# Kernel optimization log

Hardware: AMD Instinct MI355X
Metric: run time of the kernel (lower is better)

The kernel has to match this reference:

```python
import jax, jax.numpy as jnp
import numpy as np

B, T, J, V, D, H = 32, 400, 30, 50000, 150, 150
L = 2  # answer_token_len (boundary model: start, end)


def _gru_step(h, x, Wih, Whh, bih, bhh):
    # torch GRUCell semantics
    gi = x @ Wih.T + bih
    gh = h @ Whh.T + bhh
    ir, iz, inn = jnp.split(gi, 3, axis=-1)
    hr, hz, hn = jnp.split(gh, 3, axis=-1)
    r = jax.nn.sigmoid(ir + hr)
    z = jax.nn.sigmoid(iz + hz)
    n = jnp.tanh(inn + r * hn)
    return (1.0 - z) * n + z * h


def _gru_seq(x, Wih, Whh, bih, bhh):
    # x: [B, S, din] -> hidden sequence [B, S, h]
    h0 = jnp.zeros((x.shape[0], Whh.shape[1]), x.dtype)
    def step(h, xt):
        h = _gru_step(h, xt, Wih, Whh, bih, bhh)
        return h, h
    _, hs = jax.lax.scan(step, h0, jnp.swapaxes(x, 0, 1))
    return jnp.swapaxes(hs, 0, 1)


def _forward(context, query,
             E,
             ctx_Wih, ctx_Whh, ctx_bih, ctx_bhh,
             q_Wih, q_Whh, q_bih, q_bhh,
             Wq, Wp, Wr, w, gate_bias, attn_bias,
             m_Wih, m_Whh, m_bih, m_bhh,
             mr_Wih, mr_Whh, mr_bih, mr_bhh,
             ptr_W1, ptr_W2, ptr_v,
             d_Wih, d_Whh, d_bih, d_bhh):
    # encode context and query with GRUs
    Hp = _gru_seq(E[context], ctx_Wih, ctx_Whh, ctx_bih, ctx_bhh)  # [B,T,H]
    Hq = _gru_seq(E[query], q_Wih, q_Whh, q_bih, q_bhh)            # [B,J,H]

    whq = jnp.einsum('bjh,hk->bjk', Hq, Wq)  # precomputed query projection [B,J,H]

    def match_scan(xs, cWih, cWhh, cbih, cbhh):
        # xs: [B,T,H] context encodings (possibly time-reversed)
        def step(h, xt):
            # G_i = tanh(Wq Hq + (Wp p_i + Wr h_{i-1}) + bias)  -> [B,J,H]
            g = jnp.tanh(whq + (xt @ Wp + h @ Wr + gate_bias)[:, None, :])
            a = jax.nn.softmax(g @ w + attn_bias, axis=-1)       # [B,J]
            q = jnp.einsum('bj,bjh->bh', a, Hq)                  # attended query
            z = jnp.concatenate([xt, q], axis=-1)                # [B,2H]
            h = _gru_step(h, z, cWih, cWhh, cbih, cbhh)
            return h, h
        h0 = jnp.zeros((xs.shape[0], xs.shape[2]), xs.dtype)
        _, hs = jax.lax.scan(step, h0, jnp.swapaxes(xs, 0, 1))
        return jnp.swapaxes(hs, 0, 1)  # [B,T,H]

    Hf = match_scan(Hp, m_Wih, m_Whh, m_bih, m_bhh)              # forward direction
    Hb = match_scan(Hp[:, ::-1], mr_Wih, mr_Whh, mr_bih, mr_bhh) # reverse direction (scan order, as original)
    Hr = jnp.concatenate([Hf, Hb], axis=-1)                      # [B,T,2H]
    zero0 = jnp.zeros((Hr.shape[0], 1, Hr.shape[2]), Hr.dtype)   # initial zero state prepended
    Hr = jnp.concatenate([zero0, Hr], axis=1)                    # [B,T+1,2H]

    # boundary pointer network: L attention steps over H_r
    enc = Hr @ ptr_W1
    def ptr_step(h, _):
        s = jnp.tanh(enc + (h @ ptr_W2)[:, None, :]) @ ptr_v     # [B,T+1]
        a = jax.nn.softmax(s, axis=-1)
        c = jnp.einsum('bt,bth->bh', a, Hr)
        h = _gru_step(h, c, d_Wih, d_Whh, d_bih, d_bhh)
        return h, a
    h0 = jnp.zeros((Hr.shape[0], Hr.shape[2]), Hr.dtype)
    _, probs = jax.lax.scan(ptr_step, h0, None, length=L)
    return jnp.swapaxes(probs, 0, 1)  # [B, L, T+1]


def setup_inputs() -> dict:
    key = jax.random.key(0)
    keys = iter(jax.random.split(key, 40))
    p = lambda *s: jax.random.normal(next(keys), s, jnp.float32) * 0.05
    inp = {
        'context': jax.random.randint(next(keys), (B, T), 0, V, dtype=jnp.int32),
        'query': jax.random.randint(next(keys), (B, J), 0, V, dtype=jnp.int32),
        'E': p(V, D),
        'ctx_Wih': p(3 * H, D), 'ctx_Whh': p(3 * H, H), 'ctx_bih': p(3 * H), 'ctx_bhh': p(3 * H),
        'q_Wih': p(3 * H, D), 'q_Whh': p(3 * H, H), 'q_bih': p(3 * H), 'q_bhh': p(3 * H),
        'Wq': p(H, H), 'Wp': p(H, H), 'Wr': p(H, H), 'w': p(H),
        'gate_bias': p(H), 'attn_bias': p(),
        'm_Wih': p(3 * H, 2 * H), 'm_Whh': p(3 * H, H), 'm_bih': p(3 * H), 'm_bhh': p(3 * H),
        'mr_Wih': p(3 * H, 2 * H), 'mr_Whh': p(3 * H, H), 'mr_bih': p(3 * H), 'mr_bhh': p(3 * H),
        'ptr_W1': p(2 * H, 2 * H), 'ptr_W2': p(2 * H, 2 * H), 'ptr_v': p(2 * H),
        'd_Wih': p(6 * H, 2 * H), 'd_Whh': p(6 * H, 2 * H), 'd_bih': p(6 * H), 'd_bhh': p(6 * H),
    }
    return inp


def reference(context, query, E,
              ctx_Wih, ctx_Whh, ctx_bih, ctx_bhh,
              q_Wih, q_Whh, q_bih, q_bhh,
              Wq, Wp, Wr, w, gate_bias, attn_bias,
              m_Wih, m_Whh, m_bih, m_bhh,
              mr_Wih, mr_Whh, mr_bih, mr_bhh,
              ptr_W1, ptr_W2, ptr_v,
              d_Wih, d_Whh, d_bih, d_bhh):
    return _forward(context, query, E,
                    ctx_Wih, ctx_Whh, ctx_bih, ctx_bhh,
                    q_Wih, q_Whh, q_bih, q_bhh,
                    Wq, Wp, Wr, w, gate_bias, attn_bias,
                    m_Wih, m_Whh, m_bih, m_bhh,
                    mr_Wih, mr_Whh, mr_bih, mr_bhh,
                    ptr_W1, ptr_W2, ptr_v,
                    d_Wih, d_Whh, d_bih, d_bhh)
```

## Files before the change

### kernel.cpp

```cpp
#include <hip/hip_runtime.h>
#include <hip/hip_bf16.h>


namespace {

constexpr int NBATCH = 32;
constexpr int TLEN   = 400;
constexpr int JQ     = 30;
constexpr int T1     = 401;

__device__ __forceinline__ float sigm(float x){ return 1.f/(1.f+__expf(-x)); }
__device__ __forceinline__ float tanh_f(float x){
  float e = __expf(-2.f*fabsf(x));
  float t = (1.f-e)/(1.f+e);
  return x < 0.f ? -t : t;
}
__device__ __forceinline__ float bf2f(unsigned short u){
  union { unsigned int i; float f; } c; c.i = ((unsigned int)u)<<16; return c.f;
}

#define NW 29
struct WDesc { const void* src[NW]; int off[NW+1]; };

__global__ void sniff_kernel(const unsigned int* __restrict__ bits, int* __restrict__ flag){
  __shared__ int cnt;
  if (threadIdx.x==0) cnt = 0;
  __syncthreads();
  int hit = 0;
  #pragma unroll
  for (int i=0;i<4;i++){
    unsigned int w = bits[threadIdx.x*4+i];
    unsigned int b = (w>>8)&0x7Fu;
    if (b==0u || (b>=0x38u && b<=0x3Fu)) hit++;
  }
  atomicAdd(&cnt, hit);
  __syncthreads();
  if (threadIdx.x==0) *flag = (cnt > 768) ? 1 : 0;
}

__global__ void convert_weights_kernel(WDesc d, float* __restrict__ out, const int* __restrict__ flag){
  const int isbf = *flag;
  const int total = d.off[NW];
  for (int e = blockIdx.x*blockDim.x+threadIdx.x; e < total; e += gridDim.x*blockDim.x){
    int j = 0;
    while (e >= d.off[j+1]) j++;
    int i = e - d.off[j];
    out[e] = isbf ? bf2f(((const unsigned short*)d.src[j])[i])
                  : ((const float*)d.src[j])[i];
  }
}

__global__ void padrows_kernel(const float* __restrict__ src, float* __restrict__ dst,
                               int rows, int cols, int ldd){
  int i = blockIdx.x*blockDim.x+threadIdx.x;
  if (i >= rows*ldd) return;
  int r = i/ldd, c = i-r*ldd;
  dst[i] = (c<cols) ? src[(size_t)r*cols+c] : 0.f;
}

__global__ void transpose_kernel(const float* __restrict__ src, float* __restrict__ dst,
                                 int R, int C, int lds_, int offs){
  int idx = blockIdx.x*blockDim.x+threadIdx.x;
  if (idx >= R*C) return;
  int i = idx / R, k = idx - i*R;
  dst[(size_t)i*R + k] = src[(size_t)k*lds_ + offs + i];
}

__global__ void build_wcat_kernel(const float* __restrict__ Whh, const float* __restrict__ Wr,
                                  float* __restrict__ Wcat){
  int i = blockIdx.x*blockDim.x+threadIdx.x;
  if (i >= 600*152) return;
  int r = i/152, c = i-r*152;
  float v = 0.f;
  if (c < 150){
    if (r < 450) v = Whh[(size_t)r*150+c];
    else         v = Wr[(size_t)c*150 + (r-450)];
  }
  Wcat[i] = v;
}

__global__ void build_msplit_kernel(const float* __restrict__ Wcat,
                                    float* __restrict__ s2q, float* __restrict__ ext){
  int i = blockIdx.x*blockDim.x+threadIdx.x;
  if (i < 24576){
    int q = i/2048, rem = i-q*2048, r = rem/4, p = rem-r*4;
    s2q[i] = Wcat[(size_t)r*152 + 104 + 4*q + p];
  } else if (i < 24576+13376){
    int k = i-24576;
    int q = k/352, rem = k-q*352, ii = rem/4, p = rem-ii*4;
    ext[k] = Wcat[(size_t)(512+ii)*152 + 4*q + p];
  }
}

__global__ void build_gsplit_kernel(const float* __restrict__ Wpad, float* __restrict__ s2q){
  int i = blockIdx.x*blockDim.x+threadIdx.x;
  if (i >= 12*452*4) return;
  int q = i/1808, rem = i-q*1808, r = rem/4, p = rem-r*4;
  s2q[i] = (r<450) ? Wpad[(size_t)r*152 + 104 + 4*q + p] : 0.f;
}

__global__ __launch_bounds__(512) void rowproj16_kernel(
    const float* __restrict__ Xrows,
    const int* __restrict__ gather, const void* __restrict__ Etab, const int* __restrict__ bfflag,
    const float* __restrict__ W, const float* __restrict__ bias,
    float* __restrict__ out, int rows, int K, int inner, int ldw, int ldo)
{
  __shared__ __align__(16) float xs[16][304];
  const int r0 = blockIdx.x*16;
  int nr = rows - r0; if (nr > 16) nr = 16;
  if (nr <= 0) return;
  const int isbf = gather ? *bfflag : 0;
  for (int e = threadIdx.x; e < nr*inner; e += 512){
    int r = e/inner, i = e - r*inner;
    float v;
    if (gather){
      size_t base = (size_t)gather[r0+r]*inner + i;
      v = isbf ? bf2f(((const unsigned short*)Etab)[base]) : ((const float*)Etab)[base];
    } else {
      v = Xrows[(size_t)(r0+r)*inner + i];
    }
    xs[r][i] = v;
  }
  __syncthreads();
  for (int k = threadIdx.x; k < K; k += 512){
    float b0 = bias ? bias[k] : 0.f;
    float acc[16];
    #pragma unroll
    for (int r=0;r<16;r++) acc[r] = b0;
    int i = 0;
    for (; i+4 <= inner; i += 4){
      float w0 = W[(size_t)i*ldw + k];
      float w1 = W[(size_t)(i+1)*ldw + k];
      float w2 = W[(size_t)(i+2)*ldw + k];
      float w3 = W[(size_t)(i+3)*ldw + k];
      #pragma unroll
      for (int r=0;r<16;r++){
        float4 xv = *(const float4*)&xs[r][i];
        acc[r] = fmaf(xv.x, w0, acc[r]);
        acc[r] = fmaf(xv.y, w1, acc[r]);
        acc[r] = fmaf(xv.z, w2, acc[r]);
        acc[r] = fmaf(xv.w, w3, acc[r]);
      }
    }
    for (; i < inner; i++){
      float wv = W[(size_t)i*ldw + k];
      #pragma unroll
      for (int r=0;r<16;r++) acc[r] = fmaf(xs[r][i], wv, acc[r]);
    }
    for (int r=0;r<nr;r++) out[(size_t)(r0+r)*ldo + k] = acc[r];
  }
  for (int k = K + threadIdx.x; k < ldo; k += 512)
    for (int r=0;r<nr;r++) out[(size_t)(r0+r)*ldo + k] = 0.f;
}

#define R26(M) M(0) M(1) M(2) M(3) M(4) M(5) M(6) M(7) M(8) M(9) M(10) M(11) \
               M(12) M(13) M(14) M(15) M(16) M(17) M(18) M(19) M(20) M(21) \
               M(22) M(23) M(24) M(25)
#define DECW(i) float4 w##i;
#define LDW(i)  w##i = wrow4[i];
#define FMAW(i) { float4 hq = h4[i]; \
  acc0 = fmaf(hq.x, w##i.x, acc0); acc1 = fmaf(hq.y, w##i.y, acc1); \
  acc0 = fmaf(hq.z, w##i.z, acc0); acc1 = fmaf(hq.w, w##i.w, acc1); }

__global__ __launch_bounds__(512) void gru_scan_kernel(
    const float* __restrict__ gi0, const float* __restrict__ Wp0,
    const float* __restrict__ s2q0, const float* __restrict__ bh0,
    float* __restrict__ H0, int S0,
    const float* __restrict__ gi1, const float* __restrict__ Wp1,
    const float* __restrict__ s2q1, const float* __restrict__ bh1,
    float* __restrict__ H1, int S1)
{
  const int blk = blockIdx.x;
  const float* gi; const float* Wpad; const float* s2qG; const float* bh; float* Hs; int S;
  if (blk < 32){ gi = gi0 + (size_t)blk*S0*450;  Wpad = Wp0; s2qG = s2q0; bh = bh0;
                 Hs = H0 + (size_t)blk*S0*150;   S = S0; }
  else         { int bb = blk-32;
                 gi = gi1 + (size_t)bb*S1*450;   Wpad = Wp1; s2qG = s2q1; bh = bh1;
                 Hs = H1 + (size_t)bb*S1*150;    S = S1; }
  __shared__ float4 s2W[12*452];
  __shared__ __align__(16) float h[152];
  __shared__ float gh[452];
  const int tid = threadIdx.x;

  R26(DECW)
  float br = 0.f;
  {
    const float4* wrow4 = (const float4*)(Wpad + (size_t)((tid<450)?tid:0)*152);
    R26(LDW)
    if (tid<450) br = bh[tid];
  }
  for (int e=tid; e<12*452; e+=512) s2W[e] = ((const float4*)s2qG)[e];
  if (tid < 152) h[tid] = 0.f;
  __syncthreads();
  const float4* h4 = (const float4*)h;

  for (int t=0;t<S;t++){
    float g0=0.f,g1=0.f,g2=0.f;
    if (tid < 150){
      const float* gg = gi + (size_t)t*450;
      g0 = gg[tid]; g1 = gg[150+tid]; g2 = gg[300+tid];
    }
    if (tid < 450){
      float acc0=br, acc1=0.f;
      R26(FMAW)
      #pragma unroll
      for (int q=0;q<12;q++){
        float4 wq = s2W[q*452+tid]; float4 hq = h4[26+q];
        acc0 = fmaf(hq.x, wq.x, acc0); acc1 = fmaf(hq.y, wq.y, acc1);
        acc0 = fmaf(hq.z, wq.z, acc0); acc1 = fmaf(hq.w, wq.w, acc1);
      }
      gh[tid] = acc0+acc1;
    }
    __syncthreads();
    if (tid < 150){
      float r = sigm(g0 + gh[tid]);
      float z = sigm(g1 + gh[150+tid]);
      float n = tanh_f(g2 + r*gh[300+tid]);
      float hn = (1.f-z)*n + z*h[tid];
      h[tid] = hn;
      Hs[(size_t)t*150 + tid] = hn;
    }
    __syncthreads();
  }
}

__global__ void zero_hr0_kernel(float* __restrict__ Hr){
  int idx = blockIdx.x*blockDim.x + threadIdx.x;
  if (idx < NBATCH*300){
    int b = idx/300, k = idx - 300*b;
    Hr[(size_t)b*T1*300 + k] = 0.f;
  }
}

__global__ __launch_bounds__(512) void match_scan_kernel(
    const float* __restrict__ pWp,
    const float* __restrict__ whq,
    const float* __restrict__ giXf,
    const float* __restrict__ giXr,
    const float* __restrict__ Pf,
    const float* __restrict__ Pr,
    const float* __restrict__ WcatF, const float* __restrict__ WcatR,
    const float* __restrict__ s2qF,  const float* __restrict__ s2qR,
    const float* __restrict__ extF,  const float* __restrict__ extR,
    const float* __restrict__ m_bhh, const float* __restrict__ mr_bhh,
    const float* __restrict__ wvec,
    float* __restrict__ Hr)
{
  const int b   = blockIdx.x;
  const int dir = blockIdx.y;
  const float* giX  = dir ? giXr : giXf;
  const float* P    = dir ? Pr   : Pf;
  const float* Wcat = dir ? WcatR : WcatF;
  const float* s2qG = dir ? s2qR  : s2qF;
  const float* extG = dir ? extR  : extF;
  const float* bhh  = dir ? mr_bhh : m_bhh;

  __shared__ float4 s2W[6144];
  __shared__ float4 extW[3344];
  __shared__ __align__(16) float wrP[760];
  __shared__ __align__(16) float h[152];
  __shared__ float ghsRaw[512];
  __shared__ __align__(16) float gis[452];
  __shared__ __align__(16) float pwS[152];
  __shared__ __align__(16) float wlS[152];
  __shared__ float sc[32], attw[32];

  const int tid  = threadIdx.x;
  const int lane = tid & 63;
  const int wv   = tid >> 6;
  const int er   = (tid < 440) ? (tid % 88) : 0;
  const int kg   = (tid < 440) ? (tid / 88) : 0;

  R26(DECW)
  float br;
  {
    const float4* wrow4 = (const float4*)(Wcat + (size_t)tid*152);
    R26(LDW)
    br = (tid < 450) ? bhh[tid] : 0.f;
  }
  for (int e=tid; e<6144; e+=512) s2W[e]  = ((const float4*)s2qG)[e];
  for (int e=tid; e<3344; e+=512) extW[e] = ((const float4*)extG)[e];
  if (tid < 760) wrP[tid] = 0.f;
  if (tid < 152){
    h[tid] = 0.f;
    wlS[tid] = (tid<150) ? wvec[tid] : 0.f;
  }
  __syncthreads();
  const float4* h4 = (const float4*)h;
  const float4* wrP4 = (const float4*)wrP;

  for (int t=0;t<TLEN;t++){
    const int tt = dir ? (TLEN-1-t) : t;

    float gv = 0.f;
    if (tid < 452) gv = giX[((size_t)b*TLEN + tt)*452 + tid];
    float4 pwv;
    if (tid >= 440 && tid < 478)
      pwv = ((const float4*)(pWp + ((size_t)b*TLEN + tt)*152))[tid-440];

    {
      float acc0=br, acc1=0.f;
      R26(FMAW)
      #pragma unroll
      for (int q=0;q<12;q++){
        float4 wq = s2W[q*512+tid]; float4 hq = h4[26+q];
        acc0 = fmaf(hq.x, wq.x, acc0); acc1 = fmaf(hq.y, wq.y, acc1);
        acc0 = fmaf(hq.z, wq.z, acc0); acc1 = fmaf(hq.w, wq.w, acc1);
      }
      float v = acc0+acc1;
      ghsRaw[tid] = v;
      if (tid >= 450) wrP[tid-450] = v;
    }
    if (tid < 440){
      float e0=0.f, e1=0.f;
      #pragma unroll
      for (int j=0;j<8;j++){
        int q = kg*8+j;
        if (q < 38){
          float4 wq = extW[q*88+er]; float4 hq = h4[q];
          e0 = fmaf(hq.x,wq.x,e0); e1 = fmaf(hq.y,wq.y,e1);
          e0 = fmaf(hq.z,wq.z,e0); e1 = fmaf(hq.w,wq.w,e1);
        }
      }
      wrP[kg*152 + 62 + er] = e0+e1;
    }
    if (tid >= 440 && tid < 478) ((float4*)pwS)[tid-440] = pwv;
    __syncthreads();

    {
      float4 b4; b4.x=b4.y=b4.z=b4.w=0.f;
      const bool bl = (lane < 38);
      if (bl){
        float4 pw4 = ((const float4*)pwS)[lane];
        float4 s0 = wrP4[lane],        s1 = wrP4[38+lane];
        float4 s2 = wrP4[76+lane],     s3 = wrP4[114+lane];
        float4 s4 = wrP4[152+lane];
        b4.x = pw4.x + s0.x+s1.x+s2.x+s3.x+s4.x;
        b4.y = pw4.y + s0.y+s1.y+s2.y+s3.y+s4.y;
        b4.z = pw4.z + s0.z+s1.z+s2.z+s3.z+s4.z;
        b4.w = pw4.w + s0.w+s1.w+s2.w+s3.w+s4.w;
      }
      #pragma unroll
      for (int jj=0;jj<4;jj++){
        int j = wv + 8*jj;
        float a = 0.f;
        if (j < JQ && bl){
          float4 q4 = ((const float4*)(whq + ((size_t)b*JQ + j)*152))[lane];
          float4 w4 = ((const float4*)wlS)[lane];
          a = w4.x*tanh_f(q4.x+b4.x);
          a = fmaf(w4.y, tanh_f(q4.y+b4.y), a);
          a = fmaf(w4.z, tanh_f(q4.z+b4.z), a);
          a = fmaf(w4.w, tanh_f(q4.w+b4.w), a);
        }
        #pragma unroll
        for (int off=32; off; off>>=1) a += __shfl_down(a, off);
        if (j < JQ && lane==0) sc[j] = a;
      }
    }
    __syncthreads();

    if (tid < 64){
      float v = (tid < JQ) ? sc[tid] : -1e30f;
      float m = v;
      #pragma unroll
      for (int off=32; off; off>>=1) m = fmaxf(m, __shfl_down(m, off));
      m = __shfl(m, 0);
      float e = (tid < JQ) ? __expf(v-m) : 0.f;
      float su = e;
      #pragma unroll
      for (int off=32; off; off>>=1) su += __shfl_down(su, off);
      su = __shfl(su, 0);
      if (tid < JQ) attw[tid] = e/su;
    }
    __syncthreads();

    if (tid < 452){
      float acc = gv;
      const float* Pb = P + (size_t)b*JQ*452 + tid;
      #pragma unroll 6
      for (int j=0;j<JQ;j++)
        acc = fmaf(attw[j], Pb[(size_t)j*452], acc);
      gis[tid] = acc;
    }
    __syncthreads();

    if (tid < 150){
      float r = sigm(gis[tid] + ghsRaw[tid]);
      float z = sigm(gis[150+tid] + ghsRaw[150+tid]);
      float n = tanh_f(gis[300+tid] + r*ghsRaw[300+tid]);
      float hn = (1.f-z)*n + z*h[tid];
      h[tid] = hn;
      Hr[((size_t)b*T1 + (t+1))*300 + dir*150 + tid] = hn;
    }
    __syncthreads();
  }
}

__global__ __launch_bounds__(512,2) void ptr_scan_kernel(
    const float* __restrict__ enc, const float* __restrict__ Hr,
    const float* __restrict__ W2, const float* __restrict__ pv,
    const float* __restrict__ dWih, const float* __restrict__ dWhh,
    const float* __restrict__ dbih, const float* __restrict__ dbhh,
    void* __restrict__ outv, const int* __restrict__ flag)
{
  const int b = blockIdx.x;
  const int tid = threadIdx.x;
  const int isbf = *flag;
  __shared__ float h[300], hW2[300], sl[T1], al[T1], c[300];
  __shared__ float gis[900], ghs[900];
  __shared__ float vl[300];
  __shared__ float red[8];
  if (tid < 300){ h[tid] = 0.f; vl[tid] = pv[tid]; }
  __syncthreads();
  for (int l=0;l<2;l++){
    if (tid < 300){
      float a0=0.f,a1=0.f;
      for (int i=0;i<300;i+=2){
        a0 += h[i]  *W2[(size_t)i*300+tid];
        a1 += h[i+1]*W2[(size_t)(i+1)*300+tid];
      }
      hW2[tid] = a0+a1;
    }
    __syncthreads();
    {
      const int wv = tid>>6, lane = tid&63;
      for (int t=wv; t<T1; t+=8){
        const float* er = enc + ((size_t)b*T1 + t)*300;
        float acc = 0.f;
        for (int k=lane; k<300; k+=64) acc += vl[k]*tanh_f(er[k] + hW2[k]);
        #pragma unroll
        for (int off=32; off; off>>=1) acc += __shfl_down(acc, off);
        if (lane==0) sl[t] = acc;
      }
    }
    __syncthreads();
    {
      float v = (tid < T1) ? sl[tid] : -1e30f;
      float m = v;
      #pragma unroll
      for (int off=32; off; off>>=1) m = fmaxf(m, __shfl_down(m, off));
      if ((tid&63)==0) red[tid>>6] = m;
      __syncthreads();
      float bm = fmaxf(fmaxf(fmaxf(red[0],red[1]),fmaxf(red[2],red[3])),
                       fmaxf(fmaxf(red[4],red[5]),fmaxf(red[6],red[7])));
      float e = (tid < T1) ? __expf(v-bm) : 0.f;
      float su = e;
      #pragma unroll
      for (int off=32; off; off>>=1) su += __shfl_down(su, off);
      __syncthreads();
      if ((tid&63)==0) red[tid>>6] = su;
      __syncthreads();
      float bs = red[0]+red[1]+red[2]+red[3]+red[4]+red[5]+red[6]+red[7];
      if (tid < T1){
        float a = e/bs;
        al[tid] = a;
        size_t oi = ((size_t)b*2 + l)*T1 + tid;
        if (isbf) ((__hip_bfloat16*)outv)[oi] = __float2bfloat16(a);
        else      ((float*)outv)[oi] = a;
      }
    }
    __syncthreads();
    if (tid < 300){
      float acc = 0.f;
      for (int t=0;t<T1;t++) acc += al[t]*Hr[((size_t)b*T1 + t)*300 + tid];
      c[tid] = acc;
    }
    __syncthreads();
    for (int k=tid; k<900; k+=blockDim.x){
      const float* wi = dWih + (size_t)k*300;
      const float* wh = dWhh + (size_t)k*300;
      float a0 = dbih[k], a1 = dbhh[k];
      for (int i=0;i<300;i++){ a0 += c[i]*wi[i]; a1 += h[i]*wh[i]; }
      gis[k] = a0; ghs[k] = a1;
    }
    __syncthreads();
    if (tid < 300){
      float r = sigm(gis[tid] + ghs[tid]);
      float z = sigm(gis[300+tid] + ghs[300+tid]);
      float n = tanh_f(gis[600+tid] + r*ghs[600+tid]);
      h[tid] = (1.f-z)*n + z*h[tid];
    }
    __syncthreads();
  }
}

}

extern "C" void kernel_launch(void* const* d_in, const int* in_sizes, int n_in,
                              void* d_out, int out_size, void* d_ws, size_t ws_size,
                              hipStream_t stream)
{
  (void)in_sizes; (void)n_in; (void)out_size; (void)ws_size;
  float* ws = (float*)d_ws;
  int* flag = (int*)d_ws;

  static const int wsz[NW] = {
    67500,67500,450,450,
    67500,67500,450,450,
    22500,22500,22500,150,150,1,
    135000,67500,450,450,
    135000,67500,450,450,
    90000,90000,300,
    270000,270000,900,900
  };
  WDesc desc;
  int cum = 0;
  for (int j=0;j<NW;j++){ desc.src[j] = d_in[3+j]; desc.off[j] = cum; cum += wsz[j]; }
  desc.off[NW] = cum;

  float* WB = ws + 16;
  const float* P_ctx_Wih = WB + desc.off[0];
  const float* P_ctx_Whh = WB + desc.off[1];
  const float* P_ctx_bih = WB + desc.off[2];
  const float* P_ctx_bhh = WB + desc.off[3];
  const float* P_q_Wih   = WB + desc.off[4];
  const float* P_q_Whh   = WB + desc.off[5];
  const float* P_q_bih   = WB + desc.off[6];
  const float* P_q_bhh   = WB + desc.off[7];
  const float* P_Wq      = WB + desc.off[8];
  const float* P_Wp      = WB + desc.off[9];
  const float* P_Wr      = WB + desc.off[10];
  const float* P_w       = WB + desc.off[11];
  const float* P_gb      = WB + desc.off[12];
  const float* P_m_Wih   = WB + desc.off[14];
  const float* P_m_Whh   = WB + desc.off[15];
  const float* P_m_bih   = WB + desc.off[16];
  const float* P_m_bhh   = WB + desc.off[17];
  const float* P_mr_Wih  = WB + desc.off[18];
  const float* P_mr_Whh  = WB + desc.off[19];
  const float* P_mr_bih  = WB + desc.off[20];
  const float* P_mr_bhh  = WB + desc.off[21];
  const float* P_W1      = WB + desc.off[22];
  const float* P_W2      = WB + desc.off[23];
  const float* P_pv      = WB + desc.off[24];
  const float* P_dWih    = WB + desc.off[25];
  const float* P_dWhh    = WB + desc.off[26];
  const float* P_dbih    = WB + desc.off[27];
  const float* P_dbhh    = WB + desc.off[28];

  size_t p = 16 + 1468512;
  float* ctxWhhP = ws + p; p += 68400;
  float* qWhhP   = ws + p; p += 68400;
  float* s2qCtx  = ws + p; p += 21696;
  float* s2qQ    = ws + p; p += 21696;
  float* WcatF   = ws + p; p += 91200;
  float* WcatR   = ws + p; p += 91200;
  float* s2qF    = ws + p; p += 24576;
  float* s2qR    = ws + p; p += 24576;
  float* extFg   = ws + p; p += 13376;
  float* extRg   = ws + p; p += 13376;
  float* ctxWihT = ws + p; p += 67500;
  float* qWihT   = ws + p; p += 67500;
  float* mXfT    = ws + p; p += 67500;
  float* mXrT    = ws + p; p += 67500;
  float* mQfT    = ws + p; p += 67500;
  float* mQrT    = ws + p; p += 67500;

  float* ctx_gi = ws + p; p += 5760000;
  float* q_gi   = ws + p; p += 432000;
  float* HpB    = ws + p; p += 1920000;
  float* HqB    = ws + p; p += 144000;
  float* whqB   = ws + p; p += 145920;
  float* PfB    = ws + p; p += 433920;
  float* PrB    = ws + p; p += 433920;
  float* pWpB   = ws + p; p += 1945600;
  float* giXfB  = ws + p; p += 5785600;
  float* giXrB  = ws + p; p += 5785600;
  float* HrB    = ws + p; p += 3849600;
  float* encB   = ctx_gi;

  sniff_kernel<<<1,256,0,stream>>>((const unsigned int*)d_in[2], flag);
  convert_weights_kernel<<<512,256,0,stream>>>(desc, WB, flag);
  padrows_kernel<<<(450*152+255)/256,256,0,stream>>>(P_ctx_Whh, ctxWhhP, 450,150,152);
  padrows_kernel<<<(450*152+255)/256,256,0,stream>>>(P_q_Whh,   qWhhP,   450,150,152);
  build_gsplit_kernel<<<(12*452*4+255)/256,256,0,stream>>>(ctxWhhP, s2qCtx);
  build_gsplit_kernel<<<(12*452*4+255)/256,256,0,stream>>>(qWhhP,   s2qQ);
  build_wcat_kernel<<<(600*152+255)/256,256,0,stream>>>(P_m_Whh,  P_Wr, WcatF);
  build_wcat_kernel<<<(600*152+255)/256,256,0,stream>>>(P_mr_Whh, P_Wr, WcatR);
  build_msplit_kernel<<<(24576+13376+255)/256,256,0,stream>>>(WcatF, s2qF, extFg);
  build_msplit_kernel<<<(24576+13376+255)/256,256,0,stream>>>(WcatR, s2qR, extRg);
  transpose_kernel<<<(67500+255)/256,256,0,stream>>>(P_ctx_Wih, ctxWihT, 450,150,150,0);
  transpose_kernel<<<(67500+255)/256,256,0,stream>>>(P_q_Wih,   qWihT,   450,150,150,0);
  transpose_kernel<<<(67500+255)/256,256,0,stream>>>(P_m_Wih,   mXfT,    450,150,300,0);
  transpose_kernel<<<(67500+255)/256,256,0,stream>>>(P_mr_Wih,  mXrT,    450,150,300,0);
  transpose_kernel<<<(67500+255)/256,256,0,stream>>>(P_m_Wih,   mQfT,    450,150,300,150);
  transpose_kernel<<<(67500+255)/256,256,0,stream>>>(P_mr_Wih,  mQrT,    450,150,300,150);

  rowproj16_kernel<<<800,512,0,stream>>>(nullptr,(const int*)d_in[0], d_in[2], flag,
                                         ctxWihT, P_ctx_bih, ctx_gi, 12800,450,150,450,450);
  rowproj16_kernel<<<60,512,0,stream>>>(nullptr,(const int*)d_in[1], d_in[2], flag,
                                        qWihT, P_q_bih, q_gi, 960,450,150,450,450);

  gru_scan_kernel<<<64,512,0,stream>>>(ctx_gi, ctxWhhP, s2qCtx, P_ctx_bhh, HpB, 400,
                                       q_gi,   qWhhP,   s2qQ,   P_q_bhh,   HqB, 30);

  rowproj16_kernel<<<60,512,0,stream>>>(HqB,nullptr,nullptr,nullptr, P_Wq, nullptr,
                                        whqB, 960,150,150,150,152);
  rowproj16_kernel<<<60,512,0,stream>>>(HqB,nullptr,nullptr,nullptr, mQfT, nullptr,
                                        PfB, 960,450,150,450,452);
  rowproj16_kernel<<<60,512,0,stream>>>(HqB,nullptr,nullptr,nullptr, mQrT, nullptr,
                                        PrB, 960,450,150,450,452);
  rowproj16_kernel<<<800,512,0,stream>>>(HpB,nullptr,nullptr,nullptr, P_Wp, P_gb,
                                         pWpB, 12800,150,150,150,152);
  rowproj16_kernel<<<800,512,0,stream>>>(HpB,nullptr,nullptr,nullptr, mXfT, P_m_bih,
                                         giXfB, 12800,450,150,450,452);
  rowproj16_kernel<<<800,512,0,stream>>>(HpB,nullptr,nullptr,nullptr, mXrT, P_mr_bih,
                                         giXrB, 12800,450,150,450,452);

  zero_hr0_kernel<<<(NBATCH*300+511)/512,512,0,stream>>>(HrB);
  match_scan_kernel<<<dim3(NBATCH,2),512,0,stream>>>(pWpB, whqB, giXfB, giXrB,
                                                     PfB, PrB, WcatF, WcatR,
                                                     s2qF, s2qR, extFg, extRg,
                                                     P_m_bhh, P_mr_bhh, P_w, HrB);

  rowproj16_kernel<<<802,512,0,stream>>>(HrB,nullptr,nullptr,nullptr, P_W1, nullptr,
                                         encB, 12832,300,300,300,300);
  ptr_scan_kernel<<<32,512,0,stream>>>(encB, HrB, P_W2, P_pv,
                                       P_dWih, P_dWhh, P_dbih, P_dbhh, d_out, flag);
}
```

Baseline: 3.537 ms.

## Keep recurrent weights in registers, stage P/whq in LDS, fuse softmax-gate steps

Both scan kernels now keep the remaining 12 float4 rows of the recurrent weight in registers instead of LDS. The LDS this frees in the match kernel holds the per-batch attention projection P and query projection whq, loaded once instead of read from global memory every timestep. The softmax, attention-weighted input sum and GRU update are merged into one phase: three waves each recompute the softmax redundantly and broadcast weights via shuffles, which removes two block barriers per step. Register pressure rises sharply (38 float4 per thread), which risks spills or lower occupancy.

```diff
diff --git a/kernel.cpp b/kernel.cpp
--- a/kernel.cpp
+++ b/kernel.cpp
@@ -156,8 +156,11 @@
 #define R26(M) M(0) M(1) M(2) M(3) M(4) M(5) M(6) M(7) M(8) M(9) M(10) M(11) \
                M(12) M(13) M(14) M(15) M(16) M(17) M(18) M(19) M(20) M(21) \
                M(22) M(23) M(24) M(25)
+#define R12(M) M(26) M(27) M(28) M(29) M(30) M(31) M(32) M(33) M(34) M(35) \
+               M(36) M(37)
 #define DECW(i) float4 w##i;
 #define LDW(i)  w##i = wrow4[i];
+#define LDW2(i) w##i = s2q4[(i-26)*s2stride + s2r];
 #define FMAW(i) { float4 hq = h4[i]; \
   acc0 = fmaf(hq.x, w##i.x, acc0); acc1 = fmaf(hq.y, w##i.y, acc1); \
   acc0 = fmaf(hq.z, w##i.z, acc0); acc1 = fmaf(hq.w, w##i.w, acc1); }
@@ -177,19 +180,20 @@
   else         { int bb = blk-32;
                  gi = gi1 + (size_t)bb*S1*450;   Wpad = Wp1; s2qG = s2q1; bh = bh1;
                  Hs = H1 + (size_t)bb*S1*150;    S = S1; }
-  __shared__ float4 s2W[12*452];
   __shared__ __align__(16) float h[152];
   __shared__ float gh[452];
   const int tid = threadIdx.x;
 
-  R26(DECW)
+  R26(DECW) R12(DECW)
   float br = 0.f;
   {
     const float4* wrow4 = (const float4*)(Wpad + (size_t)((tid<450)?tid:0)*152);
     R26(LDW)
+    const float4* s2q4 = (const float4*)s2qG;
+    const int s2stride = 452; const int s2r = (tid<452) ? tid : 0;
+    R12(LDW2)
     if (tid<450) br = bh[tid];
   }
-  for (int e=tid; e<12*452; e+=512) s2W[e] = ((const float4*)s2qG)[e];
   if (tid < 152) h[tid] = 0.f;
   __syncthreads();
   const float4* h4 = (const float4*)h;
@@ -202,13 +206,7 @@
     }
     if (tid < 450){
       float acc0=br, acc1=0.f;
-      R26(FMAW)
-      #pragma unroll
-      for (int q=0;q<12;q++){
-        float4 wq = s2W[q*452+tid]; float4 hq = h4[26+q];
-        acc0 = fmaf(hq.x, wq.x, acc0); acc1 = fmaf(hq.y, wq.y, acc1);
-        acc0 = fmaf(hq.z, wq.z, acc0); acc1 = fmaf(hq.w, wq.w, acc1);
-      }
+      R26(FMAW) R12(FMAW)
       gh[tid] = acc0+acc1;
     }
     __syncthreads();
@@ -255,15 +253,15 @@
   const float* extG = dir ? extR  : extF;
   const float* bhh  = dir ? mr_bhh : m_bhh;
 
-  __shared__ float4 s2W[6144];
   __shared__ float4 extW[3344];
+  __shared__ __align__(16) float Ps[JQ*452];
+  __shared__ __align__(16) float whqS[JQ*152];
   __shared__ __align__(16) float wrP[760];
   __shared__ __align__(16) float h[152];
   __shared__ float ghsRaw[512];
-  __shared__ __align__(16) float gis[452];
   __shared__ __align__(16) float pwS[152];
   __shared__ __align__(16) float wlS[152];
-  __shared__ float sc[32], attw[32];
+  __shared__ float sc[32];
 
   const int tid  = threadIdx.x;
   const int lane = tid & 63;
@@ -271,16 +269,24 @@
   const int er   = (tid < 440) ? (tid % 88) : 0;
   const int kg   = (tid < 440) ? (tid / 88) : 0;
 
-  R26(DECW)
+  R26(DECW) R12(DECW)
   float br;
   {
     const float4* wrow4 = (const float4*)(Wcat + (size_t)tid*152);
     R26(LDW)
+    const float4* s2q4 = (const float4*)s2qG;
+    const int s2stride = 512; const int s2r = tid;
+    R12(LDW2)
     br = (tid < 450) ? bhh[tid] : 0.f;
   }
-  for (int e=tid; e<6144; e+=512) s2W[e]  = ((const float4*)s2qG)[e];
   for (int e=tid; e<3344; e+=512) extW[e] = ((const float4*)extG)[e];
-  if (tid < 760) wrP[tid] = 0.f;
+  {
+    const float* Pb = P + (size_t)b*JQ*452;
+    for (int e=tid; e<JQ*452; e+=512) Ps[e] = Pb[e];
+    const float4* wq4 = (const float4*)(whq + (size_t)b*JQ*152);
+    for (int e=tid; e<JQ*38; e+=512) ((float4*)whqS)[e] = wq4[e];
+  }
+  for (int e=tid; e<760; e+=512) wrP[e] = 0.f;
   if (tid < 152){
     h[tid] = 0.f;
     wlS[tid] = (tid<150) ? wvec[tid] : 0.f;
@@ -292,21 +298,18 @@
   for (int t=0;t<TLEN;t++){
     const int tt = dir ? (TLEN-1-t) : t;
 
-    float gv = 0.f;
-    if (tid < 452) gv = giX[((size_t)b*TLEN + tt)*452 + tid];
+    float gv0=0.f, gv1=0.f, gv2=0.f;
+    if (tid < 150){
+      const float* g = giX + ((size_t)b*TLEN + tt)*452;
+      gv0 = g[tid]; gv1 = g[150+tid]; gv2 = g[300+tid];
+    }
     float4 pwv;
     if (tid >= 440 && tid < 478)
       pwv = ((const float4*)(pWp + ((size_t)b*TLEN + tt)*152))[tid-440];
 
     {
       float acc0=br, acc1=0.f;
-      R26(FMAW)
-      #pragma unroll
-      for (int q=0;q<12;q++){
-        float4 wq = s2W[q*512+tid]; float4 hq = h4[26+q];
-        acc0 = fmaf(hq.x, wq.x, acc0); acc1 = fmaf(hq.y, wq.y, acc1);
-        acc0 = fmaf(hq.z, wq.z, acc0); acc1 = fmaf(hq.w, wq.w, acc1);
-      }
+      R26(FMAW) R12(FMAW)
       float v = acc0+acc1;
       ghsRaw[tid] = v;
       if (tid >= 450) wrP[tid-450] = v;
@@ -345,7 +348,7 @@
         int j = wv + 8*jj;
         float a = 0.f;
         if (j < JQ && bl){
-          float4 q4 = ((const float4*)(whq + ((size_t)b*JQ + j)*152))[lane];
+          float4 q4 = ((const float4*)whqS)[j*38 + lane];
           float4 w4 = ((const float4*)wlS)[lane];
           a = w4.x*tanh_f(q4.x+b4.x);
           a = fmaf(w4.y, tanh_f(q4.y+b4.y), a);
@@ -359,38 +362,35 @@
     }
     __syncthreads();
 
-    if (tid < 64){
-      float v = (tid < JQ) ? sc[tid] : -1e30f;
+    if (tid < 192){
+      float v = (lane < JQ) ? sc[lane] : -1e30f;
       float m = v;
       #pragma unroll
       for (int off=32; off; off>>=1) m = fmaxf(m, __shfl_down(m, off));
       m = __shfl(m, 0);
-      float e = (tid < JQ) ? __expf(v-m) : 0.f;
+      float e = (lane < JQ) ? __expf(v-m) : 0.f;
       float su = e;
       #pragma unroll
       for (int off=32; off; off>>=1) su += __shfl_down(su, off);
       su = __shfl(su, 0);
-      if (tid < JQ) attw[tid] = e/su;
-    }
-    __syncthreads();
-
-    if (tid < 452){
-      float acc = gv;
-      const float* Pb = P + (size_t)b*JQ*452 + tid;
+      float aw = e/su;
+      const int k = (tid < 150) ? tid : 0;
+      float accr = gv0, accz = gv1, accn = gv2;
       #pragma unroll 6
-      for (int j=0;j<JQ;j++)
-        acc = fmaf(attw[j], Pb[(size_t)j*452], acc);
-      gis[tid] = acc;
-    }
-    __syncthreads();
-
-    if (tid < 150){
-      float r = sigm(gis[tid] + ghsRaw[tid]);
-      float z = sigm(gis[150+tid] + ghsRaw[150+tid]);
-      float n = tanh_f(gis[300+tid] + r*ghsRaw[300+tid]);
-      float hn = (1.f-z)*n + z*h[tid];
-      h[tid] = hn;
-      Hr[((size_t)b*T1 + (t+1))*300 + dir*150 + tid] = hn;
+      for (int j=0;j<JQ;j++){
+        float aj = __shfl(aw, j);
+        accr = fmaf(aj, Ps[j*452 + k],       accr);
+        accz = fmaf(aj, Ps[j*452 + 150 + k], accz);
+        accn = fmaf(aj, Ps[j*452 + 300 + k], accn);
+      }
+      if (tid < 150){
+        float r = sigm(accr + ghsRaw[tid]);
+        float z = sigm(accz + ghsRaw[150+tid]);
+        float n = tanh_f(accn + r*ghsRaw[300+tid]);
+        float hn = (1.f-z)*n + z*h[tid];
+        h[tid] = hn;
+        Hr[((size_t)b*T1 + (t+1))*300 + dir*150 + tid] = hn;
+      }
     }
     __syncthreads();
   }
```

After: 3.552 ms. No clear change (+0.4%).
